# Kernel tuning notes

Hardware: AMD Instinct MI355X
Metric: run time of the kernel (lower is better)

The kernel has to match this reference:

```python
import jax, jax.numpy as jnp
import numpy as np

N_USERS = 60000
N_ITEMS = 40000
D = 64
N_BEH = 3
L_GLOBAL = 2
L_SINGLE = 2
E_GLOBAL = 1_000_000
E_BEH = 500_000
BATCH = 4096
REG_WEIGHT = 1e-3
DIM_QK = 64
N_NODES = N_USERS + 1 + N_ITEMS + 1
USER_GLOBAL_W = 2.35
USER_BEH_W = 0.242
ITEM_GLOBAL_W = 1.0
ITEM_BEH_W = 0.55


def setup_inputs() -> dict:
    key = jax.random.key(0)
    ks = jax.random.split(key, 9)
    user_emb = (jax.random.normal(ks[0], (N_USERS + 1, D), jnp.float32) * 0.1).at[0].set(0.0)
    item_emb = (jax.random.normal(ks[1], (N_ITEMS + 1, D), jnp.float32) * 0.1).at[0].set(0.0)
    w_scale = 1.0 / np.sqrt(D)
    global_W = jax.random.normal(ks[2], (L_GLOBAL, D, D), jnp.float32) * w_scale
    global_b = jnp.zeros((L_GLOBAL, D), jnp.float32)
    beh_W = jax.random.normal(ks[3], (N_BEH, L_SINGLE, D, D), jnp.float32) * w_scale
    beh_b = jnp.zeros((N_BEH, L_SINGLE, D), jnp.float32)
    all_edge_index = jax.random.randint(ks[4], (2, E_GLOBAL), 0, N_NODES, jnp.int32)
    beh_edge_index = jax.random.randint(ks[5], (N_BEH, 2, E_BEH), 0, N_NODES, jnp.int32)
    batch_data = jax.random.randint(ks[6], (BATCH, N_BEH, 3), 0, N_ITEMS + 1, jnp.int32)
    return {
        "user_emb": user_emb, "item_emb": item_emb,
        "global_W": global_W, "global_b": global_b,
        "beh_W": beh_W, "beh_b": beh_b,
        "all_edge_index": all_edge_index, "beh_edge_index": beh_edge_index,
        "batch_data": batch_data,
    }


def _gcn_conv(h, src, dst, W, b):
    # PyG GCNConv, add_self_loops=False: out[dst] += d^-1/2[src] d^-1/2[dst] (h W)[src] + b
    N = h.shape[0]
    hw = h @ W
    deg = jnp.zeros((N,), hw.dtype).at[dst].add(1.0)
    dinv = jnp.where(deg > 0, jax.lax.rsqrt(jnp.maximum(deg, 1.0)), 0.0)
    coef = (dinv[src] * dinv[dst])[:, None]          # [E,1]
    out = jax.ops.segment_sum(hw[src] * coef, dst, num_segments=N)
    return out + b


def _graph_encoder(x, edge_index, Ws, bs):
    src, dst = edge_index[0], edge_index[1]
    res = x
    h = x
    for i in range(Ws.shape[0]):
        h = _gcn_conv(h, src, dst, Ws[i], bs[i])
        h = h / jnp.maximum(jnp.linalg.norm(h, axis=-1, keepdims=True), 1e-12)  # F.normalize
        res = res + h / (i + 1.0)
    return res


def _mutual_attention(tok):
    # tok: [N, B, D]; per-node BxB softmax attention
    scale = 1.0 / np.sqrt(DIM_QK)
    att = jax.nn.softmax(jnp.einsum('nbd,ncd->nbc', tok, tok) * scale, axis=-1)
    return jnp.einsum('nbc,ncd->nbd', att, tok)


def reference(user_emb, item_emb, global_W, global_b, beh_W, beh_b,
              all_edge_index, beh_edge_index, batch_data):
    nu = user_emb.shape[0]
    all_emb = jnp.concatenate([user_emb, item_emb], axis=0)        # [N, D]
    all_emb = _graph_encoder(all_emb, all_edge_index, global_W, global_b)
    u_g, i_g = all_emb[:nu], all_emb[nu:]
    beh_u, beh_i = [], []
    for b_idx in range(N_BEH):
        e = _graph_encoder(all_emb, beh_edge_index[b_idx], beh_W[b_idx], beh_b[b_idx])
        beh_u.append(e[:nu])
        beh_i.append(e[nu:])
    all_u = jnp.stack(beh_u, axis=1)                               # [nu, B, D]
    all_i = jnp.stack(beh_i, axis=1)                               # [ni, B, D]
    all_u = _mutual_attention(all_u)
    all_i = _mutual_attention(all_i)
    uw = USER_GLOBAL_W * u_g[:, None, :] + USER_BEH_W * all_u      # [nu, B, D]
    iw = ITEM_GLOBAL_W * i_g[:, None, :] + ITEM_BEH_W * all_i      # [ni, B, D]

    total = jnp.float32(0.0)
    for i in range(N_BEH):
        data = batch_data[:, i]
        users = data[:, 0]
        items = data[:, 1:]                                        # [batch, 2]
        uf = uw[:, i][users][:, None, :]                           # [batch, 1, D]
        for j in range(N_BEH):
            itf = iw[:, j][items]                                  # [batch, 2, D]
            scores = jnp.sum(uf * itf, axis=2)                     # [batch, 2]
            total = total - jnp.mean(jax.nn.log_sigmoid(scores[:, 0] - scores[:, 1]))
    emb_loss = (jnp.linalg.norm(user_emb) + jnp.linalg.norm(item_emb)) / item_emb.shape[0]
    return total + REG_WEIGHT * emb_loss
```

## Files before the change

### kernel.cpp

```cpp
#include <hip/hip_runtime.h>
#include <math.h>

#define NU 60001
#define NI 40001
#define NN 100002
#define EG 1000000
#define EB 500000
#define BATCH 4096
#define WNODE 12501
#define EC 36
#define ECR 20
#define SENTB (NN * 64)

typedef float floatx2 __attribute__((ext_vector_type(2)));
typedef short bf16x8 __attribute__((ext_vector_type(8)));
typedef float f32x4 __attribute__((ext_vector_type(4)));

__device__ inline float wave_sum(float v) {
#pragma unroll
  for (int off = 32; off > 0; off >>= 1) v += __shfl_down(v, off);
  return __shfl(v, 0);
}

__device__ inline float sub_sum16(float v) {
#pragma unroll
  for (int off = 8; off > 0; off >>= 1) v += __shfl_xor(v, off);
  return v;
}

__device__ inline float dot4(float4 a, float4 b) {
  return fmaf(a.x, b.x, fmaf(a.y, b.y, fmaf(a.z, b.z, a.w * b.w)));
}

__device__ inline unsigned short f2b(float f) {
  unsigned u = __float_as_uint(f);
  return (unsigned short)((u + 0x7fffu + ((u >> 16) & 1u)) >> 16);
}
__device__ inline float b2f(unsigned short h) {
  return __uint_as_float((unsigned)h << 16);
}
__device__ inline float4 ld4b(const unsigned short* p) {
  ushort4 u = *(const ushort4*)p;
  return make_float4(b2f(u.x), b2f(u.y), b2f(u.z), b2f(u.w));
}
__device__ inline unsigned pack2b(float a, float b) {
  return (unsigned)f2b(a) | ((unsigned)f2b(b) << 16);
}

__device__ inline unsigned char f2fp8(float f) {
  return (unsigned char)(__builtin_amdgcn_cvt_pk_fp8_f32(f, f, 0, false) & 0xff);
}
__device__ inline unsigned int pack4_fp8(float4 v) {
  int pk = __builtin_amdgcn_cvt_pk_fp8_f32(v.x, v.y, 0, false);
  pk = __builtin_amdgcn_cvt_pk_fp8_f32(v.z, v.w, pk, true);
  return (unsigned int)pk;
}

__global__ void k_bucket(const int* __restrict__ eg, const int* __restrict__ eb,
                         int* __restrict__ cnt, int* __restrict__ e16,
                         int* __restrict__ edgr) {
  int set = blockIdx.y;
  int win = blockIdx.x & 7;
  int chunk = blockIdx.x >> 3;
  int E = set ? EB : EG;
  int base0 = chunk * 1024;
  if (base0 >= E) return;
  const int* sp = set ? (eb + (long)(set - 1) * 2 * EB) : eg;
  int lo = win * WNODE;
  int hi = min(NN, lo + WNODE);
  int base = base0 + threadIdx.x;
#pragma unroll
  for (int j = 0; j < 4; j++) {
    int e = base + j * 256;
    if (e < E) {
      int d = sp[E + e];
      if (d >= lo && d < hi) {
        int s = sp[e];
        int pos = atomicAdd(cnt + set * NN + d, 1);
        if (pos < 16) e16[((long)set * NN + d) * 16 + pos] = s << 6;
        else if (pos < EC) edgr[((long)set * NN + d) * ECR + (pos - 16)] = s << 6;
      }
    }
  }
}

__global__ void k_prep(const int* __restrict__ cnt, float* __restrict__ dinv,
                       const float* __restrict__ gW, const float* __restrict__ bW,
                       unsigned short* __restrict__ wt,
                       unsigned char* __restrict__ tbsb, unsigned char* __restrict__ asg,
                       unsigned char* __restrict__ asb) {
  const long NEp = (long)(NN + 1) * 64;
  int i = blockIdx.x * blockDim.x + threadIdx.x;
  if (i < 4 * NN) {
    int c = cnt[i];
    dinv[i] = (c > 0) ? rsqrtf((float)c) : 0.f;
  }
  if (i < 8 * 4096) {
    int m = i >> 12, idx = i & 4095;
    int col = idx >> 6, k = idx & 63;
    const float* src = (m < 2) ? (gW + m * 4096) : (bW + (long)(m - 2) * 4096);
    wt[i] = f2b(src[k * 64 + col]);
  }
  if (i < 448) {
    int row = i >> 6, b = i & 63;
    if (row < 3) tbsb[row * NEp + SENTB + b] = 0;
    else if (row == 3) asg[SENTB + b] = 0;
    else asb[(row - 4) * NEp + SENTB + b] = 0;
  }
}

__global__ void k_tbs0(const float4* __restrict__ ue, const float4* __restrict__ ie,
                       const float* __restrict__ dinv, unsigned int* __restrict__ out) {
  long i = (long)blockIdx.x * blockDim.x + threadIdx.x;
  if (i >= (long)(NN + 1) * 16) return;
  int row = (int)(i >> 4);
  if (row >= NN) { out[i] = 0; return; }
  float4 v = (row < NU) ? ue[i] : ie[i - (long)NU * 16];
  float dv = dinv[row];
  v.x *= dv; v.y *= dv; v.z *= dv; v.w *= dv;
  out[i] = pack4_fp8(v);
}

#define CVTA(r)                                       \
  a0 += __builtin_amdgcn_cvt_pk_f32_fp8(r.x, false);  \
  a1 += __builtin_amdgcn_cvt_pk_f32_fp8(r.x, true);   \
  a2 += __builtin_amdgcn_cvt_pk_f32_fp8(r.y, false);  \
  a3 += __builtin_amdgcn_cvt_pk_f32_fp8(r.y, true);

#define CVTB(r)                                       \
  b0 += __builtin_amdgcn_cvt_pk_f32_fp8(r.x, false);  \
  b1 += __builtin_amdgcn_cvt_pk_f32_fp8(r.x, true);   \
  b2 += __builtin_amdgcn_cvt_pk_f32_fp8(r.y, false);  \
  b3 += __builtin_amdgcn_cvt_pk_f32_fp8(r.y, true);

template <int MODE>
__global__ void __launch_bounds__(256, 8) k_gcn(
    const unsigned char* __restrict__ tb, const int* __restrict__ e16,
    const int* __restrict__ edgr,
    const int* __restrict__ cnt, const float* __restrict__ dinv,
    const unsigned short* __restrict__ Wt, const float* __restrict__ biasb,
    const float* __restrict__ basef, const float* __restrict__ base2f,
    const unsigned short* __restrict__ base16,
    unsigned short* __restrict__ res16, unsigned char* __restrict__ outS,
    unsigned char* __restrict__ tbs123) {
  __shared__ __align__(16) short accs[32][72];
  __shared__ float ssq[32][2];
  const long NE = (long)NN * 64;
  const long NEp = (long)(NN + 1) * 64;

  int t = threadIdx.x;
  int w = t >> 6, lane = t & 63;
  int sub3 = lane >> 3, sl8 = lane & 7;
  int sub = lane >> 4, sl16 = lane & 15;
  int set = blockIdx.y;

  const float* bias;
  if (MODE <= 1) bias = biasb;
  else bias = biasb + set * 128 + (MODE == 3 ? 64 : 0);
  const unsigned short* wt = Wt + ((MODE >= 2) ? (long)set * 8192 : 0);
  int cs = (MODE >= 2) ? (1 + set) : 0;
  const unsigned char* tbl = (MODE >= 2) ? tb + (long)set * NEp : tb;
  unsigned char* outp = (MODE == 2) ? outS + (long)set * NEp : outS;

  int tilebase = (w >> 1) << 4;
  int cg = (w & 1) << 5;
  int ncolA = cg + sl16, ncolB = cg + 16 + sl16;

  int nb0 = blockIdx.x * 32;
  int node = nb0 + (w << 3) + sub3;
  bool vn = node < NN;
  long nid = (long)cs * NN + (vn ? node : 0);
  const int* ep = e16 + nid * 16;
  int4 e0 = *(const int4*)(ep);
  int4 e1 = *(const int4*)(ep + 4);
  int4 e2 = *(const int4*)(ep + 8);
  int4 e3 = *(const int4*)(ep + 12);
  int deg = vn ? min(cnt[cs * NN + node], EC) : 0;
  float dvn = vn ? dinv[cs * NN + node] : 0.f;
  int mx = deg;
  mx = max(mx, __shfl_xor(mx, 8));
  mx = max(mx, __shfl_xor(mx, 16));
  mx = max(mx, __shfl_xor(mx, 32));

  int ls = sl8 << 3;
  floatx2 a0 = {0.f, 0.f}, a1 = {0.f, 0.f}, a2 = {0.f, 0.f}, a3 = {0.f, 0.f};
  floatx2 b0 = {0.f, 0.f}, b1 = {0.f, 0.f}, b2 = {0.f, 0.f}, b3 = {0.f, 0.f};
  {
    int o0 = (0 < deg) ? e0.x : SENTB;
    int o1 = (1 < deg) ? e0.y : SENTB;
    int o2 = (2 < deg) ? e0.z : SENTB;
    int o3 = (3 < deg) ? e0.w : SENTB;
    int o4 = (4 < deg) ? e1.x : SENTB;
    int o5 = (5 < deg) ? e1.y : SENTB;
    int o6 = (6 < deg) ? e1.z : SENTB;
    int o7 = (7 < deg) ? e1.w : SENTB;
    int o8 = (8 < deg) ? e2.x : SENTB;
    int o9 = (9 < deg) ? e2.y : SENTB;
    int o10 = (10 < deg) ? e2.z : SENTB;
    int o11 = (11 < deg) ? e2.w : SENTB;
    int o12 = (12 < deg) ? e3.x : SENTB;
    int o13 = (13 < deg) ? e3.y : SENTB;
    int o14 = (14 < deg) ? e3.z : SENTB;
    int o15 = (15 < deg) ? e3.w : SENTB;
    uint2 r0 = *(const uint2*)(tbl + o0 + ls);
    uint2 r1 = *(const uint2*)(tbl + o1 + ls);
    uint2 r2 = *(const uint2*)(tbl + o2 + ls);
    uint2 r3 = *(const uint2*)(tbl + o3 + ls);
    uint2 r4 = *(const uint2*)(tbl + o4 + ls);
    uint2 r5 = *(const uint2*)(tbl + o5 + ls);
    uint2 r6 = *(const uint2*)(tbl + o6 + ls);
    uint2 r7 = *(const uint2*)(tbl + o7 + ls);
    uint2 r8 = *(const uint2*)(tbl + o8 + ls);
    uint2 r9 = *(const uint2*)(tbl + o9 + ls);
    uint2 r10 = *(const uint2*)(tbl + o10 + ls);
    uint2 r11 = *(const uint2*)(tbl + o11 + ls);
    uint2 r12 = *(const uint2*)(tbl + o12 + ls);
    uint2 r13 = *(const uint2*)(tbl + o13 + ls);
    uint2 r14 = *(const uint2*)(tbl + o14 + ls);
    uint2 r15 = *(const uint2*)(tbl + o15 + ls);
    CVTA(r0); CVTA(r1); CVTA(r2); CVTA(r3);
    CVTA(r4); CVTA(r5); CVTA(r6); CVTA(r7);
    CVTB(r8); CVTB(r9); CVTB(r10); CVTB(r11);
    CVTB(r12); CVTB(r13); CVTB(r14); CVTB(r15);
  }
  const int* epr = edgr + nid * ECR;
  for (int ch = 16; ch < mx; ch += 8) {
    int rem = deg - ch;
    int4 f0 = *(const int4*)(epr + (ch - 16));
    int4 f1 = *(const int4*)(epr + (ch - 16) + 4);
    int o0 = (0 < rem) ? f0.x : SENTB;
    int o1 = (1 < rem) ? f0.y : SENTB;
    int o2 = (2 < rem) ? f0.z : SENTB;
    int o3 = (3 < rem) ? f0.w : SENTB;
    int o4 = (4 < rem) ? f1.x : SENTB;
    int o5 = (5 < rem) ? f1.y : SENTB;
    int o6 = (6 < rem) ? f1.z : SENTB;
    int o7 = (7 < rem) ? f1.w : SENTB;
    uint2 r0 = *(const uint2*)(tbl + o0 + ls);
    uint2 r1 = *(const uint2*)(tbl + o1 + ls);
    uint2 r2 = *(const uint2*)(tbl + o2 + ls);
    uint2 r3 = *(const uint2*)(tbl + o3 + ls);
    uint2 r4 = *(const uint2*)(tbl + o4 + ls);
    uint2 r5 = *(const uint2*)(tbl + o5 + ls);
    uint2 r6 = *(const uint2*)(tbl + o6 + ls);
    uint2 r7 = *(const uint2*)(tbl + o7 + ls);
    CVTA(r0); CVTA(r1); CVTA(r2); CVTA(r3);
    CVTB(r4); CVTB(r5); CVTB(r6); CVTB(r7);
  }
  a0 += b0; a1 += b1; a2 += b2; a3 += b3;
  floatx2 dv2 = {dvn, dvn};
  a0 *= dv2; a1 *= dv2; a2 *= dv2; a3 *= dv2;
  int4 pk4;
  pk4.x = (int)pack2b(a0.x, a0.y);
  pk4.y = (int)pack2b(a1.x, a1.y);
  pk4.z = (int)pack2b(a2.x, a2.y);
  pk4.w = (int)pack2b(a3.x, a3.y);
  *(int4*)&accs[(w << 3) + sub3][sl8 << 3] = pk4;

  bf16x8 bfA0 = *(const bf16x8*)(wt + ncolA * 64 + (sub << 3));
  bf16x8 bfA1 = *(const bf16x8*)(wt + ncolA * 64 + 32 + (sub << 3));
  bf16x8 bfB0 = *(const bf16x8*)(wt + ncolB * 64 + (sub << 3));
  bf16x8 bfB1 = *(const bf16x8*)(wt + ncolB * 64 + 32 + (sub << 3));
  float biasA = bias[ncolA], biasB = bias[ncolB];
  __syncthreads();

  int arow = tilebase + sl16;
  bf16x8 fa0 = *(const bf16x8*)&accs[arow][sub << 3];
  bf16x8 fa1 = *(const bf16x8*)&accs[arow][32 + (sub << 3)];
  f32x4 cA = {0.f, 0.f, 0.f, 0.f}, cB = {0.f, 0.f, 0.f, 0.f};
  cA = __builtin_amdgcn_mfma_f32_16x16x32_bf16(fa0, bfA0, cA, 0, 0, 0);
  cA = __builtin_amdgcn_mfma_f32_16x16x32_bf16(fa1, bfA1, cA, 0, 0, 0);
  cB = __builtin_amdgcn_mfma_f32_16x16x32_bf16(fa0, bfB0, cB, 0, 0, 0);
  cB = __builtin_amdgcn_mfma_f32_16x16x32_bf16(fa1, bfB1, cB, 0, 0, 0);

  float vA[4], vB[4];
#pragma unroll
  for (int r = 0; r < 4; r++) { vA[r] = cA[r] + biasA; vB[r] = cB[r] + biasB; }
#pragma unroll
  for (int r = 0; r < 4; r++) {
    float p = sub_sum16(fmaf(vA[r], vA[r], vB[r] * vB[r]));
    if (sl16 == 0) ssq[tilebase + (sub << 2) + r][w & 1] = p;
  }
  __syncthreads();
#pragma unroll
  for (int r = 0; r < 4; r++) {
    int nl = tilebase + (sub << 2) + r;
    float ss = ssq[nl][0] + ssq[nl][1];
    float inv = 1.0f / fmaxf(sqrtf(ss), 1e-12f);
    float hA = vA[r] * inv, hB = vB[r] * inv;
    int gn = nb0 + nl;
    if (gn < NN) {
      long iA = (long)gn * 64 + ncolA, iB = (long)gn * 64 + ncolB;
      float dv = dinv[cs * NN + gn];
      if (MODE == 0 || MODE == 2) {
        outp[iA] = f2fp8(hA * dv);
        outp[iB] = f2fp8(hB * dv);
      } else if (MODE == 1) {
        float idv = (dv > 0.f) ? 1.0f / dv : 0.f;
        float ownA = __builtin_amdgcn_cvt_f32_fp8((unsigned int)tbl[iA], 0) * idv;
        float ownB = __builtin_amdgcn_cvt_f32_fp8((unsigned int)tbl[iB], 0) * idv;
        float bA, bB;
        if (gn < NU) { bA = basef[iA]; bB = basef[iB]; }
        else {
          long o2 = (long)(gn - NU) * 64;
          bA = base2f[o2 + ncolA]; bB = base2f[o2 + ncolB];
        }
        float rA = bA + ownA + 0.5f * hA, rB = bB + ownB + 0.5f * hB;
        res16[iA] = f2b(rA); res16[iB] = f2b(rB);
#pragma unroll
        for (int k = 0; k < 3; k++) {
          float dk = dinv[(1 + k) * NN + gn];
          tbs123[(long)k * NEp + iA] = f2fp8(rA * dk);
          tbs123[(long)k * NEp + iB] = f2fp8(rB * dk);
        }
      } else {
        float idv = (dv > 0.f) ? 1.0f / dv : 0.f;
        float ownA = __builtin_amdgcn_cvt_f32_fp8((unsigned int)tbl[iA], 0) * idv;
        float ownB = __builtin_amdgcn_cvt_f32_fp8((unsigned int)tbl[iB], 0) * idv;
        float rA = b2f(base16[iA]) + ownA + 0.5f * hA;
        float rB = b2f(base16[iB]) + ownB + 0.5f * hB;
        (res16 + (long)set * NE)[iA] = f2b(rA);
        (res16 + (long)set * NE)[iB] = f2b(rB);
      }
    }
  }
}

__device__ inline void item_iw4(const unsigned short* __restrict__ G,
                                const unsigned short* __restrict__ B0,
                                const unsigned short* __restrict__ B1,
                                const unsigned short* __restrict__ B2,
                                long o, float4& iw0, float4& iw1, float4& iw2) {
  float4 g = ld4b(G + o);
  float4 t0 = ld4b(B0 + o);
  float4 t1 = ld4b(B1 + o);
  float4 t2 = ld4b(B2 + o);
  float g00 = sub_sum16(dot4(t0, t0)), g01 = sub_sum16(dot4(t0, t1));
  float g02 = sub_sum16(dot4(t0, t2)), g11 = sub_sum16(dot4(t1, t1));
  float g12 = sub_sum16(dot4(t1, t2)), g22 = sub_sum16(dot4(t2, t2));
  const float S = 0.125f;
  float gm[3][3] = {{g00, g01, g02}, {g01, g11, g12}, {g02, g12, g22}};
  float4* out[3] = {&iw0, &iw1, &iw2};
#pragma unroll
  for (int j = 0; j < 3; j++) {
    float a0 = gm[j][0] * S, a1 = gm[j][1] * S, a2 = gm[j][2] * S;
    float m = fmaxf(a0, fmaxf(a1, a2));
    float e0 = expf(a0 - m), e1 = expf(a1 - m), e2 = expf(a2 - m);
    float inv = 1.f / (e0 + e1 + e2);
    float w0 = e0 * inv, w1 = e1 * inv, w2 = e2 * inv;
    float4 r;
    r.x = fmaf(0.55f, w0 * t0.x + w1 * t1.x + w2 * t2.x, g.x);
    r.y = fmaf(0.55f, w0 * t0.y + w1 * t1.y + w2 * t2.y, g.y);
    r.z = fmaf(0.55f, w0 * t0.z + w1 * t1.z + w2 * t2.z, g.z);
    r.w = fmaf(0.55f, w0 * t0.w + w1 * t1.w + w2 * t2.w, g.w);
    *out[j] = r;
  }
}

__global__ void __launch_bounds__(256) k_loss(
    const unsigned short* __restrict__ G, const unsigned short* __restrict__ B0,
    const unsigned short* __restrict__ B1, const unsigned short* __restrict__ B2,
    const int* __restrict__ batch, float* __restrict__ acc) {
  int tid = blockIdx.x * blockDim.x + threadIdx.x;
  int lane = tid & 63;
  int sub = lane >> 4, sl = lane & 15;
  int task = (tid >> 6) * 4 + sub;
  if (task >= BATCH * 3) return;
  int i = task % 3;
  const int* bd = batch + (long)task * 3;
  int u = bd[0], p = bd[1], q = bd[2];

  float4 uf;
  {
    long o = (long)u * 64 + sl * 4;
    float4 g = ld4b(G + o);
    float4 t0 = ld4b(B0 + o);
    float4 t1 = ld4b(B1 + o);
    float4 t2 = ld4b(B2 + o);
    float4 ti = (i == 0) ? t0 : ((i == 1) ? t1 : t2);
    float a0 = sub_sum16(dot4(ti, t0)) * 0.125f;
    float a1 = sub_sum16(dot4(ti, t1)) * 0.125f;
    float a2 = sub_sum16(dot4(ti, t2)) * 0.125f;
    float m = fmaxf(a0, fmaxf(a1, a2));
    float e0 = expf(a0 - m), e1 = expf(a1 - m), e2 = expf(a2 - m);
    float inv = 1.f / (e0 + e1 + e2);
    float w0 = e0 * inv, w1 = e1 * inv, w2 = e2 * inv;
    uf.x = fmaf(2.35f, g.x, 0.242f * (w0 * t0.x + w1 * t1.x + w2 * t2.x));
    uf.y = fmaf(2.35f, g.y, 0.242f * (w0 * t0.y + w1 * t1.y + w2 * t2.y));
    uf.z = fmaf(2.35f, g.z, 0.242f * (w0 * t0.z + w1 * t1.z + w2 * t2.z));
    uf.w = fmaf(2.35f, g.w, 0.242f * (w0 * t0.w + w1 * t1.w + w2 * t2.w));
  }

  float4 p0, p1, p2, q0, q1, q2;
  item_iw4(G, B0, B1, B2, ((long)(NU + p)) * 64 + sl * 4, p0, p1, p2);
  item_iw4(G, B0, B1, B2, ((long)(NU + q)) * 64 + sl * 4, q0, q1, q2);

  float sp0 = sub_sum16(dot4(uf, p0)), sq0 = sub_sum16(dot4(uf, q0));
  float sp1 = sub_sum16(dot4(uf, p1)), sq1 = sub_sum16(dot4(uf, q1));
  float sp2 = sub_sum16(dot4(uf, p2)), sq2 = sub_sum16(dot4(uf, q2));

  if (sl == 0) {
    float loc = 0.f;
    float xs[3] = {sp0 - sq0, sp1 - sq1, sp2 - sq2};
#pragma unroll
    for (int j = 0; j < 3; j++) {
      float x = xs[j];
      loc += fminf(x, 0.f) - log1pf(expf(-fabsf(x)));
    }
    atomicAdd(acc, loc);
  }
}

__global__ void k_sumsq(const float* __restrict__ x, long n, float* __restrict__ acc) {
  long stride = (long)gridDim.x * blockDim.x;
  float v = 0.f;
  for (long i = (long)blockIdx.x * blockDim.x + threadIdx.x; i < n; i += stride) {
    float t = x[i];
    v = fmaf(t, t, v);
  }
  v = wave_sum(v);
  if ((threadIdx.x & 63) == 0) atomicAdd(acc, v);
}

__global__ void k_final(const float* __restrict__ acc, float* __restrict__ out) {
  out[0] = -acc[0] * (1.0f / (float)BATCH) +
           0.001f * ((sqrtf(acc[1]) + sqrtf(acc[2])) / (float)NI);
}

extern "C" void kernel_launch(void* const* d_in, const int* in_sizes, int n_in,
                              void* d_out, int out_size, void* d_ws, size_t ws_size,
                              hipStream_t stream) {
  const float* ue = (const float*)d_in[0];
  const float* ie = (const float*)d_in[1];
  const float* gW = (const float*)d_in[2];
  const float* gb = (const float*)d_in[3];
  const float* bW = (const float*)d_in[4];
  const float* bb = (const float*)d_in[5];
  const int* eg = (const int*)d_in[6];
  const int* eb = (const int*)d_in[7];
  const int* batch = (const int*)d_in[8];
  float* out = (float*)d_out;

  const long NE = (long)NN * 64;
  const long NEp = (long)(NN + 1) * 64;
  unsigned short* G16 = (unsigned short*)d_ws;
  unsigned short* B16 = G16 + NE;
  float* DINV = (float*)(B16 + 3 * NE);
  float* ACC = DINV + 4 * NN;
  int* CNT = (int*)(ACC + 8);
  unsigned short* WT = (unsigned short*)(CNT + 4 * NN);
  int* E16 = (int*)(WT + 8 * 4096);
  int* EDGR = E16 + 4L * NN * 16;
  unsigned char* TBS0 = (unsigned char*)(EDGR + 4L * NN * ECR + 8);
  unsigned char* TBSb = TBS0 + NEp;
  unsigned char* ASg = TBSb + 3 * NEp;
  unsigned char* ASb = ASg + NEp;

  hipMemsetAsync(ACC, 0, 8 * sizeof(float), stream);
  hipMemsetAsync(CNT, 0, 4 * NN * sizeof(int), stream);

  const int GB = (NN + 31) / 32;

  k_bucket<<<dim3(8 * ((EG + 1023) / 1024), 4), 256, 0, stream>>>(
      eg, eb, CNT, E16, EDGR);

  k_prep<<<(4 * NN + 255) / 256, 256, 0, stream>>>(CNT, DINV, gW, bW, WT,
                                                   TBSb, ASg, ASb);
  k_tbs0<<<(int)(((NN + 1) * 16 + 255) / 256), 256, 0, stream>>>(
      (const float4*)ue, (const float4*)ie, DINV, (unsigned int*)TBS0);

  k_gcn<0><<<dim3(GB, 1), 256, 0, stream>>>(TBS0, E16, EDGR, CNT, DINV, WT, gb,
                                            nullptr, nullptr, nullptr, nullptr,
                                            ASg, nullptr);
  k_gcn<1><<<dim3(GB, 1), 256, 0, stream>>>(ASg, E16, EDGR, CNT, DINV, WT + 4096,
                                            gb + 64, ue, ie, nullptr, G16,
                                            nullptr, TBSb);

  k_gcn<2><<<dim3(GB, 3), 256, 0, stream>>>(TBSb, E16, EDGR, CNT, DINV, WT + 8192,
                                            bb, nullptr, nullptr, nullptr,
                                            nullptr, ASb, nullptr);
  k_gcn<3><<<dim3(GB, 3), 256, 0, stream>>>(ASb, E16, EDGR, CNT, DINV, WT + 12288,
                                            bb, nullptr, nullptr, G16, B16,
                                            nullptr, nullptr);

  k_loss<<<(BATCH * 3) / 16, 256, 0, stream>>>(G16, B16, B16 + NE, B16 + 2 * NE,
                                               batch, ACC);

  k_sumsq<<<512, 256, 0, stream>>>(ue, (long)NU * 64, ACC + 1);
  k_sumsq<<<512, 256, 0, stream>>>(ie, (long)NI * 64, ACC + 2);

  k_final<<<1, 1, 0, stream>>>(ACC, out);
}
```

Before: 471.1 us.

## Make edge bucketing persistent with XCD-affine window work stealing

The bucketing kernel becomes a persistent grid of 2048 blocks. Each block reads its XCD id from a hardware register and starts on the destination-node window matching that XCD. It claims 1024-edge chunks through per-window atomic counters, then moves on to the other windows. The aim is to keep the atomics and scattered writes for a window inside one XCD's L2 and to balance load dynamically. The cost is two block-wide barriers and one global atomic per chunk claimed.

New measurement: 822.2 us. 1.75x slower.

```diff
diff --git a/kernel.cpp b/kernel.cpp
--- a/kernel.cpp
+++ b/kernel.cpp
@@ -11,6 +11,9 @@
 #define EC 36
 #define ECR 20
 #define SENTB (NN * 64)
+#define NCHUNK_G ((EG + 1023) / 1024)
+#define NCHUNK_B ((EB + 1023) / 1024)
+#define NCHUNK_TOT (NCHUNK_G + 3 * NCHUNK_B)
 
 typedef float floatx2 __attribute__((ext_vector_type(2)));
 typedef short bf16x8 __attribute__((ext_vector_type(8)));
@@ -56,29 +59,46 @@
   return (unsigned int)pk;
 }
 
-__global__ void k_bucket(const int* __restrict__ eg, const int* __restrict__ eb,
-                         int* __restrict__ cnt, int* __restrict__ e16,
-                         int* __restrict__ edgr) {
-  int set = blockIdx.y;
-  int win = blockIdx.x & 7;
-  int chunk = blockIdx.x >> 3;
-  int E = set ? EB : EG;
-  int base0 = chunk * 1024;
-  if (base0 >= E) return;
-  const int* sp = set ? (eb + (long)(set - 1) * 2 * EB) : eg;
-  int lo = win * WNODE;
-  int hi = min(NN, lo + WNODE);
-  int base = base0 + threadIdx.x;
-#pragma unroll
-  for (int j = 0; j < 4; j++) {
-    int e = base + j * 256;
-    if (e < E) {
-      int d = sp[E + e];
-      if (d >= lo && d < hi) {
-        int s = sp[e];
-        int pos = atomicAdd(cnt + set * NN + d, 1);
-        if (pos < 16) e16[((long)set * NN + d) * 16 + pos] = s << 6;
-        else if (pos < EC) edgr[((long)set * NN + d) * ECR + (pos - 16)] = s << 6;
+__global__ void __launch_bounds__(256) k_bucket(
+    const int* __restrict__ eg, const int* __restrict__ eb,
+    int* __restrict__ cnt, int* __restrict__ e16,
+    int* __restrict__ edgr, int* __restrict__ claim) {
+  int xcd;
+  asm volatile("s_getreg_b32 %0, hwreg(HW_REG_XCC_ID)" : "=s"(xcd));
+  xcd &= 7;
+  __shared__ int sc;
+  for (int k = 0; k < 8; k++) {
+    int q = (xcd + k) & 7;
+    int lo = q * WNODE;
+    int hi = min(NN, lo + WNODE);
+    for (;;) {
+      __syncthreads();
+      if (threadIdx.x == 0) sc = atomicAdd(claim + q, 1);
+      __syncthreads();
+      int c = sc;
+      if (c >= NCHUNK_TOT) break;
+      int set, chunk;
+      if (c < NCHUNK_G) { set = 0; chunk = c; }
+      else {
+        int r = c - NCHUNK_G;
+        set = 1 + r / NCHUNK_B;
+        chunk = r % NCHUNK_B;
+      }
+      int E = set ? EB : EG;
+      const int* sp = set ? (eb + (long)(set - 1) * 2 * EB) : eg;
+      int base = chunk * 1024 + threadIdx.x;
+#pragma unroll
+      for (int j = 0; j < 4; j++) {
+        int e = base + j * 256;
+        if (e < E) {
+          int d = sp[E + e];
+          if (d >= lo && d < hi) {
+            int s = sp[e];
+            int pos = atomicAdd(cnt + set * NN + d, 1);
+            if (pos < 16) e16[((long)set * NN + d) * 16 + pos] = s << 6;
+            else if (pos < EC) edgr[((long)set * NN + d) * ECR + (pos - 16)] = s << 6;
+          }
+        }
       }
     }
   }
@@ -448,7 +468,8 @@
   float* DINV = (float*)(B16 + 3 * NE);
   float* ACC = DINV + 4 * NN;
   int* CNT = (int*)(ACC + 8);
-  unsigned short* WT = (unsigned short*)(CNT + 4 * NN);
+  int* CLAIM = CNT + 4 * NN;
+  unsigned short* WT = (unsigned short*)(CLAIM + 8);
   int* E16 = (int*)(WT + 8 * 4096);
   int* EDGR = E16 + 4L * NN * 16;
   unsigned char* TBS0 = (unsigned char*)(EDGR + 4L * NN * ECR + 8);
@@ -457,12 +478,11 @@
   unsigned char* ASb = ASg + NEp;
 
   hipMemsetAsync(ACC, 0, 8 * sizeof(float), stream);
-  hipMemsetAsync(CNT, 0, 4 * NN * sizeof(int), stream);
+  hipMemsetAsync(CNT, 0, (4 * NN + 8) * sizeof(int), stream);
 
   const int GB = (NN + 31) / 32;
 
-  k_bucket<<<dim3(8 * ((EG + 1023) / 1024), 4), 256, 0, stream>>>(
-      eg, eb, CNT, E16, EDGR);
+  k_bucket<<<2048, 256, 0, stream>>>(eg, eb, CNT, E16, EDGR, CLAIM);
 
   k_prep<<<(4 * NN + 255) / 256, 256, 0, stream>>>(CNT, DINV, gW, bW, WT,
                                                    TBSb, ASg, ASb);
```
